# Kernel optimization log

Measured on AMD Instinct MI355X. Metric: run time of the kernel, lower is better.

Reference implementation:

```python
import jax, jax.numpy as jnp
import numpy as np

B, C, H, W = 8, 512, 64, 64
NUMS, V_C = 1024, 512
RATE = 0.999


def _normalize(x):
    # matches torch F.normalize(dim=-1, eps=1e-12)
    return x / jnp.clip(jnp.linalg.norm(x, axis=-1, keepdims=True), 1e-12)


def setup_inputs() -> dict:
    key = jax.random.key(0)
    k1, k2, k3 = jax.random.split(key, 3)
    return {
        "x": jax.random.normal(k1, (B, C, H, W), dtype=jnp.float32),
        "noise_feature": jax.random.normal(k2, (NUMS, C), dtype=jnp.float32),
        "std": jax.random.normal(k3, (NUMS, V_C), dtype=jnp.float32),
    }


def reference(x, noise_feature, std):
    b, c, h, w = x.shape
    # (b,c,h,w) -> (n,c)
    xf = jnp.transpose(x, (0, 2, 3, 1)).reshape(-1, c)
    m = jax.lax.stop_gradient(noise_feature)  # torch uses .data (no grad)
    xn = _normalize(xf)
    mn = _normalize(m)
    score = xn @ mn.T  # (n, k) cosine similarities

    # EMA codebook update (training path, update_flag=True)
    xd = jax.lax.stop_gradient(xf)
    embed_ind = jnp.argmax(score, axis=1)  # (n,)
    # segment_sum == x.T @ one_hot(ind), transposed; avoids dense one-hot GEMM
    embed_sum = jax.ops.segment_sum(xd, embed_ind, num_segments=NUMS)  # (k, c)
    counts = jax.ops.segment_sum(jnp.ones((xd.shape[0],), xd.dtype), embed_ind,
                                 num_segments=NUMS)  # (k,)
    embed_mean = embed_sum / (counts[:, None] + 1e-6)
    new_m = m * RATE + embed_mean * (1.0 - RATE)

    mn2 = _normalize(new_m)
    score2 = xn @ mn2.T  # (n, k)
    soft_label = jax.nn.softmax(score2, axis=1)
    out = (soft_label @ std).reshape(b, h, w, V_C)
    return out, score2
```

## Files before the change

### kernel.cpp

```cpp
#include <hip/hip_runtime.h>
#include <stdint.h>

#define NROWS 32768
#define CDIM  512
#define KCODES 1024
#define VC    512
#define LDP 72

typedef unsigned short u16;
typedef unsigned long long u64;
using bf16x8 = __attribute__((ext_vector_type(8))) __bf16;
using f32x4  = __attribute__((ext_vector_type(4))) float;

__device__ __forceinline__ float bf2f(u16 u){
  union { unsigned int i; float f; } x; x.i = ((unsigned int)u) << 16; return x.f;
}
__device__ __forceinline__ u16 f2bf(float f){
  union { float f; unsigned int i; } x; x.f = f;
  unsigned int u = x.i;
  u += 0x7fffu + ((u >> 16) & 1u);
  return (u16)(u >> 16);
}
__device__ __forceinline__ unsigned int pack2(u16 lo, u16 hi){
  return (unsigned int)lo | ((unsigned int)hi << 16);
}
__device__ __forceinline__ unsigned int fkey(float f){
  unsigned int u = __float_as_uint(f);
  return (u & 0x80000000u) ? ~u : (u | 0x80000000u);
}
__device__ __forceinline__ f32x4 mfma16(bf16x8 a, bf16x8 b, f32x4 c){
  return __builtin_amdgcn_mfma_f32_16x16x32_bf16(a, b, c, 0, 0, 0);
}
__device__ __forceinline__ void gload_lds16(const void* g, void* l){
  __builtin_amdgcn_global_load_lds(
      (const __attribute__((address_space(1))) unsigned int*)g,
      (__attribute__((address_space(3))) unsigned int*)l, 16, 0, 0);
}

__global__ __launch_bounds__(256) void k_transpose_x(const float* __restrict__ x,
                                                     u16* __restrict__ xf){
  __shared__ float tile[32][33];
  int b  = blockIdx.z;
  int p0 = blockIdx.x * 32;
  int c0 = blockIdx.y * 32;
  int tx = threadIdx.x, ty = threadIdx.y;
  const float* xb = x + (size_t)b * CDIM * 4096;
#pragma unroll
  for (int i = 0; i < 4; i++){
    int c = c0 + ty + i * 8;
    tile[ty + i * 8][tx] = xb[(size_t)c * 4096 + p0 + tx];
  }
  __syncthreads();
#pragma unroll
  for (int i = 0; i < 4; i++){
    int p = p0 + ty + i * 8;
    xf[((size_t)(b * 4096 + p)) * CDIM + c0 + tx] = f2bf(tile[tx][ty + i * 8]);
  }
}

__global__ __launch_bounds__(256) void k_rownorm(const u16* __restrict__ xf,
                                                 float* __restrict__ rinv){
  int row  = blockIdx.x * 4 + (threadIdx.x >> 6);
  int lane = threadIdx.x & 63;
  const uint4* p = (const uint4*)(xf + (size_t)row * CDIM);
  uint4 v = p[lane];
  unsigned int w[4] = {v.x, v.y, v.z, v.w};
  float s = 0.f;
#pragma unroll
  for (int i = 0; i < 4; i++){
    float a = bf2f((u16)(w[i] & 0xffffu));
    float b = bf2f((u16)(w[i] >> 16));
    s += a * a + b * b;
  }
#pragma unroll
  for (int off = 32; off; off >>= 1) s += __shfl_xor(s, off, 64);
  if (lane == 0) rinv[row] = 1.0f / fmaxf(sqrtf(s), 1e-12f);
}

__global__ __launch_bounds__(256) void k_norm_rows(const float* __restrict__ in,
                                                   u16* __restrict__ out){
  int row  = blockIdx.x * 4 + (threadIdx.x >> 6);
  int lane = threadIdx.x & 63;
  const float* r = in + (size_t)row * CDIM;
  float v[8]; float s = 0.f;
#pragma unroll
  for (int i = 0; i < 8; i++){ v[i] = r[lane + i * 64]; s += v[i] * v[i]; }
#pragma unroll
  for (int off = 32; off; off >>= 1) s += __shfl_xor(s, off, 64);
  float inv = 1.0f / fmaxf(sqrtf(s), 1e-12f);
#pragma unroll
  for (int i = 0; i < 8; i++) out[(size_t)row * CDIM + lane + i * 64] = f2bf(v[i] * inv);
}

__global__ __launch_bounds__(256) void k_transpose_std(const float* __restrict__ sd,
                                                       u16* __restrict__ stdT){
  __shared__ float tile[32][33];
  int k0 = blockIdx.x * 32;
  int v0 = blockIdx.y * 32;
  int tx = threadIdx.x, ty = threadIdx.y;
#pragma unroll
  for (int i = 0; i < 4; i++)
    tile[ty + i * 8][tx] = sd[(size_t)(k0 + ty + i * 8) * VC + v0 + tx];
  __syncthreads();
#pragma unroll
  for (int i = 0; i < 4; i++)
    stdT[(size_t)(v0 + ty + i * 8) * KCODES + k0 + tx] = f2bf(tile[tx][ty + i * 8]);
}

__global__ __launch_bounds__(256) void k_gemm1_am(const u16* __restrict__ xf,
                                                  const u16* __restrict__ mn,
                                                  u64* __restrict__ packed){
  __shared__ u16 As[128 * 64];
  __shared__ u16 Bs[128 * 64];
  int tid  = threadIdx.x;
  int wave = tid >> 6, lane = tid & 63;
  int wr = wave >> 1, wc = wave & 1;
  int quad = lane >> 4, l15 = lane & 15;
  int c0 = blockIdx.x * 128, r0 = blockIdx.y * 128;

  int srow = lane >> 3, schunk = lane & 7;
  const u16* ag = xf + (size_t)(r0 + wave * 8 + srow) * CDIM + schunk * 8;
  const u16* bg = mn + (size_t)(c0 + wave * 8 + srow) * CDIM + schunk * 8;
  u16* adst = As + wave * 8 * 64;
  u16* bdst = Bs + wave * 8 * 64;

  f32x4 acc[4][4];
#pragma unroll
  for (int rt = 0; rt < 4; rt++)
#pragma unroll
    for (int ct = 0; ct < 4; ct++) acc[rt][ct] = (f32x4)(0.f);

  for (int k0 = 0; k0 < CDIM; k0 += 64){
#pragma unroll
    for (int i = 0; i < 4; i++){
      gload_lds16(ag + (size_t)i * 32 * CDIM + k0, adst + i * 32 * 64);
      gload_lds16(bg + (size_t)i * 32 * CDIM + k0, bdst + i * 32 * 64);
    }
    __syncthreads();
#pragma unroll
    for (int ks = 0; ks < 2; ks++){
      bf16x8 af[4], bfr[4];
#pragma unroll
      for (int rt = 0; rt < 4; rt++)
        af[rt] = *(const bf16x8*)(As + (wr * 64 + rt * 16 + l15) * 64 + ks * 32 + quad * 8);
#pragma unroll
      for (int ct = 0; ct < 4; ct++)
        bfr[ct] = *(const bf16x8*)(Bs + (wc * 64 + ct * 16 + l15) * 64 + ks * 32 + quad * 8);
#pragma unroll
      for (int rt = 0; rt < 4; rt++)
#pragma unroll
        for (int ct = 0; ct < 4; ct++)
          acc[rt][ct] = mfma16(af[rt], bfr[ct], acc[rt][ct]);
    }
    __syncthreads();
  }

#pragma unroll
  for (int rt = 0; rt < 4; rt++){
#pragma unroll
    for (int q = 0; q < 4; q++){
      float bv = acc[rt][0][q];
      int   bc = c0 + wc * 64 + l15;
#pragma unroll
      for (int ct = 1; ct < 4; ct++){
        float v = acc[rt][ct][q];
        int   c = c0 + wc * 64 + ct * 16 + l15;
        if (v > bv){ bv = v; bc = c; }
      }
#pragma unroll
      for (int off = 1; off <= 8; off <<= 1){
        float ov = __shfl_xor(bv, off, 64);
        int   oc = __shfl_xor(bc, off, 64);
        if (ov > bv || (ov == bv && oc < bc)){ bv = ov; bc = oc; }
      }
      if (l15 == 0){
        int rg = r0 + wr * 64 + rt * 16 + quad * 4 + q;
        u64 key = ((u64)fkey(bv) << 32) | (unsigned int)(~(unsigned int)bc);
        atomicMax(packed + rg, key);
      }
    }
  }
}

__global__ __launch_bounds__(256) void k_decode(const u64* __restrict__ packed,
                                                int* __restrict__ ind){
  int i = blockIdx.x * 256 + threadIdx.x;
  ind[i] = (int)(~(unsigned int)(packed[i] & 0xffffffffull)) & (KCODES - 1);
}

__global__ __launch_bounds__(256) void k_gather(const int* __restrict__ ind,
                                                const u16* __restrict__ xf,
                                                float* __restrict__ esum,
                                                float* __restrict__ counts){
  __shared__ float part[4][CDIM];
  __shared__ int   wcnt[4];
  int code = blockIdx.x;
  int tid = threadIdx.x, wave = tid >> 6, lane = tid & 63;
  float acc[8] = {0,0,0,0,0,0,0,0};
  int cnt = 0;
  for (int base = wave * 64; base < NROWS; base += 256){
    int match = (ind[base + lane] == code);
    u64 mask = __ballot(match);
    cnt += (int)__popcll(mask);
    while (mask){
      int b = __ffsll((long long)mask) - 1;
      mask &= mask - 1;
      int rr = base + b;
      uint4 v = *(const uint4*)(xf + (size_t)rr * CDIM + lane * 8);
      unsigned int w[4] = {v.x, v.y, v.z, v.w};
#pragma unroll
      for (int i = 0; i < 4; i++){
        acc[2 * i]     += bf2f((u16)(w[i] & 0xffffu));
        acc[2 * i + 1] += bf2f((u16)(w[i] >> 16));
      }
    }
  }
#pragma unroll
  for (int j = 0; j < 8; j++) part[wave][lane * 8 + j] = acc[j];
  if (lane == 0) wcnt[wave] = cnt;
  __syncthreads();
  for (int c = tid; c < CDIM; c += 256)
    esum[(size_t)code * CDIM + c] = part[0][c] + part[1][c] + part[2][c] + part[3][c];
  if (tid == 0) counts[code] = (float)(wcnt[0] + wcnt[1] + wcnt[2] + wcnt[3]);
}

__global__ __launch_bounds__(256) void k_newm(const float* __restrict__ m,
                                              const float* __restrict__ esum,
                                              const float* __restrict__ counts,
                                              u16* __restrict__ mn2){
  int row  = blockIdx.x * 4 + (threadIdx.x >> 6);
  int lane = threadIdx.x & 63;
  float cnt = counts[row];
  float sc  = 0.001f / (cnt + 1e-6f);
  float v[8]; float s = 0.f;
#pragma unroll
  for (int i = 0; i < 8; i++){
    int c = lane + i * 64;
    v[i] = m[(size_t)row * CDIM + c] * 0.999f + esum[(size_t)row * CDIM + c] * sc;
    s += v[i] * v[i];
  }
#pragma unroll
  for (int off = 32; off; off >>= 1) s += __shfl_xor(s, off, 64);
  float inv = 1.0f / fmaxf(sqrtf(s), 1e-12f);
#pragma unroll
  for (int i = 0; i < 8; i++) mn2[(size_t)row * CDIM + lane + i * 64] = f2bf(v[i] * inv);
}

__global__ __launch_bounds__(256) void k_gemm2(const u16* __restrict__ xf,
                                               const u16* __restrict__ mn2,
                                               const float* __restrict__ rinv,
                                               float* __restrict__ score2,
                                               float* __restrict__ pmax,
                                               float* __restrict__ psum){
  __shared__ u16 As[128 * 64];
  __shared__ u16 Bs[128 * 64];
  int tid  = threadIdx.x;
  int wave = tid >> 6, lane = tid & 63;
  int wr = wave >> 1, wc = wave & 1;
  int quad = lane >> 4, l15 = lane & 15;
  int c0 = blockIdx.x * 128, r0 = blockIdx.y * 128;

  int srow = lane >> 3, schunk = lane & 7;
  const u16* ag = xf  + (size_t)(r0 + wave * 8 + srow) * CDIM + schunk * 8;
  const u16* bg = mn2 + (size_t)(c0 + wave * 8 + srow) * CDIM + schunk * 8;
  u16* adst = As + wave * 8 * 64;
  u16* bdst = Bs + wave * 8 * 64;

  f32x4 acc[4][4];
#pragma unroll
  for (int rt = 0; rt < 4; rt++)
#pragma unroll
    for (int ct = 0; ct < 4; ct++) acc[rt][ct] = (f32x4)(0.f);

  for (int k0 = 0; k0 < CDIM; k0 += 64){
#pragma unroll
    for (int i = 0; i < 4; i++){
      gload_lds16(ag + (size_t)i * 32 * CDIM + k0, adst + i * 32 * 64);
      gload_lds16(bg + (size_t)i * 32 * CDIM + k0, bdst + i * 32 * 64);
    }
    __syncthreads();
#pragma unroll
    for (int ks = 0; ks < 2; ks++){
      bf16x8 af[4], bfr[4];
#pragma unroll
      for (int rt = 0; rt < 4; rt++)
        af[rt] = *(const bf16x8*)(As + (wr * 64 + rt * 16 + l15) * 64 + ks * 32 + quad * 8);
#pragma unroll
      for (int ct = 0; ct < 4; ct++)
        bfr[ct] = *(const bf16x8*)(Bs + (wc * 64 + ct * 16 + l15) * 64 + ks * 32 + quad * 8);
#pragma unroll
      for (int rt = 0; rt < 4; rt++)
#pragma unroll
        for (int ct = 0; ct < 4; ct++)
          acc[rt][ct] = mfma16(af[rt], bfr[ct], acc[rt][ct]);
    }
    __syncthreads();
  }

#pragma unroll
  for (int rt = 0; rt < 4; rt++){
#pragma unroll
    for (int q = 0; q < 4; q++){
      int grow = r0 + wr * 64 + rt * 16 + quad * 4 + q;
      float rv = rinv[grow];
      float v0 = acc[rt][0][q] * rv;
      float v1 = acc[rt][1][q] * rv;
      float v2 = acc[rt][2][q] * rv;
      float v3 = acc[rt][3][q] * rv;
      float* so = score2 + (size_t)grow * KCODES + c0 + wc * 64 + l15;
      so[0]  = v0;
      so[16] = v1;
      so[32] = v2;
      so[48] = v3;
      float mx = fmaxf(fmaxf(v0, v1), fmaxf(v2, v3));
#pragma unroll
      for (int off = 1; off <= 8; off <<= 1) mx = fmaxf(mx, __shfl_xor(mx, off, 64));
      float s = __expf(v0 - mx) + __expf(v1 - mx) + __expf(v2 - mx) + __expf(v3 - mx);
#pragma unroll
      for (int off = 1; off <= 8; off <<= 1) s += __shfl_xor(s, off, 64);
      if (l15 == 0){
        int pi = grow * 16 + blockIdx.x * 2 + wc;
        pmax[pi] = mx;
        psum[pi] = s;
      }
    }
  }
}

__global__ __launch_bounds__(256) void k_softcomb(const float* __restrict__ pmax,
                                                  const float* __restrict__ psum,
                                                  float* __restrict__ rowmax,
                                                  float* __restrict__ rsinv){
  int row = blockIdx.x * 256 + threadIdx.x;
  const float* pm = pmax + (size_t)row * 16;
  const float* ps = psum + (size_t)row * 16;
  float M = pm[0];
#pragma unroll
  for (int i = 1; i < 16; i++) M = fmaxf(M, pm[i]);
  float S = 0.f;
#pragma unroll
  for (int i = 0; i < 16; i++) S += ps[i] * __expf(pm[i] - M);
  rowmax[row] = M;
  rsinv[row]  = 1.0f / S;
}

__global__ __launch_bounds__(512) void k_gemm3(const float* __restrict__ score2,
                                               const float* __restrict__ rowmax,
                                               const float* __restrict__ rsinv,
                                               const u16* __restrict__ stdT,
                                               float* __restrict__ out){
  __shared__ u16 As[128 * LDP];
  __shared__ u16 Bs[256 * 64];
  int tid  = threadIdx.x;
  int wave = tid >> 6, lane = tid & 63;
  int wr = wave >> 2, wcol = wave & 3;
  int quad = lane >> 4, l15 = lane & 15;
  int c0 = blockIdx.x * 256, r0 = blockIdx.y * 128;
  int arow = tid >> 2, aq = tid & 3;

  int srow = lane >> 3, schunk = lane & 7;
  const u16* bg = stdT + (size_t)(c0 + wave * 8 + srow) * KCODES + schunk * 8;
  u16* bdst = Bs + wave * 8 * 64;

  float rmax = rowmax[r0 + arow];
  float rs   = rsinv [r0 + arow];

  f32x4 acc[4][4];
#pragma unroll
  for (int rt = 0; rt < 4; rt++)
#pragma unroll
    for (int ct = 0; ct < 4; ct++) acc[rt][ct] = (f32x4)(0.f);

  const float* ag = score2 + (size_t)(r0 + arow) * KCODES + aq * 16;

  for (int k0 = 0; k0 < KCODES; k0 += 64){
#pragma unroll
    for (int i = 0; i < 4; i++)
      gload_lds16(bg + (size_t)i * 64 * KCODES + k0, bdst + i * 64 * 64);
#pragma unroll
    for (int j = 0; j < 2; j++){
      float4 a = *(const float4*)(ag + k0 + j * 8);
      float4 b = *(const float4*)(ag + k0 + j * 8 + 4);
      uint4 o;
      o.x = pack2(f2bf(__expf(a.x - rmax) * rs), f2bf(__expf(a.y - rmax) * rs));
      o.y = pack2(f2bf(__expf(a.z - rmax) * rs), f2bf(__expf(a.w - rmax) * rs));
      o.z = pack2(f2bf(__expf(b.x - rmax) * rs), f2bf(__expf(b.y - rmax) * rs));
      o.w = pack2(f2bf(__expf(b.z - rmax) * rs), f2bf(__expf(b.w - rmax) * rs));
      *(uint4*)(As + arow * LDP + aq * 16 + j * 8) = o;
    }
    __syncthreads();
#pragma unroll
    for (int ks = 0; ks < 2; ks++){
      bf16x8 af[4], bfr[4];
#pragma unroll
      for (int rt = 0; rt < 4; rt++)
        af[rt] = *(const bf16x8*)(As + (wr * 64 + rt * 16 + l15) * LDP + ks * 32 + quad * 8);
#pragma unroll
      for (int ct = 0; ct < 4; ct++)
        bfr[ct] = *(const bf16x8*)(Bs + (wcol * 64 + ct * 16 + l15) * 64 + ks * 32 + quad * 8);
#pragma unroll
      for (int rt = 0; rt < 4; rt++)
#pragma unroll
        for (int ct = 0; ct < 4; ct++)
          acc[rt][ct] = mfma16(af[rt], bfr[ct], acc[rt][ct]);
    }
    __syncthreads();
  }
#pragma unroll
  for (int rt = 0; rt < 4; rt++){
#pragma unroll
    for (int q = 0; q < 4; q++){
      int grow = r0 + wr * 64 + rt * 16 + quad * 4 + q;
#pragma unroll
      for (int ct = 0; ct < 4; ct++){
        int gcol = c0 + wcol * 64 + ct * 16 + l15;
        out[(size_t)grow * VC + gcol] = acc[rt][ct][q];
      }
    }
  }
}

extern "C" void kernel_launch(void* const* d_in, const int* in_sizes, int n_in,
                              void* d_out, int out_size, void* d_ws, size_t ws_size,
                              hipStream_t stream){
  (void)in_sizes; (void)n_in; (void)out_size; (void)ws_size;
  const float* x      = (const float*)d_in[0];
  const float* m      = (const float*)d_in[1];
  const float* stdmat = (const float*)d_in[2];
  float* out    = (float*)d_out;
  float* score2 = out + (size_t)NROWS * VC;

  char* ws = (char*)d_ws;
  u16*   xf     = (u16*)  (ws + 0);
  u16*   mn     = (u16*)  (ws + 33554432);
  u16*   mn2    = (u16*)  (ws + 34603008);
  u16*   stdT   = (u16*)  (ws + 35651584);
  float* rinv   = (float*)(ws + 36700160);
  u64*   packed = (u64*)  (ws + 36831232);
  int*   ind    = (int*)  (ws + 37093376);
  float* esum   = (float*)(ws + 37224448);
  float* counts = (float*)(ws + 39321600);
  float* rowmax = (float*)(ws + 39325696);
  float* rsinv  = (float*)(ws + 39456768);
  float* pmax   = (float*)(ws + 39587840);
  float* psum   = (float*)(ws + 41684992);

  hipMemsetAsync(packed, 0, (size_t)NROWS * 8, stream);

  k_transpose_x  <<<dim3(128, 16, 8), dim3(32, 8), 0, stream>>>(x, xf);
  k_rownorm      <<<NROWS / 4, 256, 0, stream>>>(xf, rinv);
  k_norm_rows    <<<KCODES / 4, 256, 0, stream>>>(m, mn);
  k_transpose_std<<<dim3(32, 16), dim3(32, 8), 0, stream>>>(stdmat, stdT);
  k_gemm1_am     <<<dim3(KCODES / 128, NROWS / 128), 256, 0, stream>>>(xf, mn, packed);
  k_decode       <<<NROWS / 256, 256, 0, stream>>>(packed, ind);
  k_gather       <<<KCODES, 256, 0, stream>>>(ind, xf, esum, counts);
  k_newm         <<<KCODES / 4, 256, 0, stream>>>(m, esum, counts, mn2);
  k_gemm2        <<<dim3(KCODES / 128, NROWS / 128), 256, 0, stream>>>(xf, mn2, rinv, score2, pmax, psum);
  k_softcomb     <<<NROWS / 256, 256, 0, stream>>>(pmax, psum, rowmax, rsinv);
  k_gemm3        <<<dim3(VC / 256, NROWS / 128), 512, 0, stream>>>(score2, rowmax, rsinv, stdT, out);
}
```

Before: 507.2 us.

## Fuse score GEMM, online softmax and value GEMM into a flash-style kernel

Replaces the separate score GEMM, softmax-combine and softmax@std GEMM kernels with one kernel per 64-row tile. The tile keeps the x rows resident in LDS, streams codebook and std chunks, and applies an online softmax with running max and sum rescaling. This avoids re-reading the 128MB score2 matrix and recomputing exp in a separate pass. The cost is about 145KB of LDS per block, which limits occupancy to one block per CU. The small per-chunk tiles (32 codes) with several barriers per iteration may also underuse the MFMA units.

```diff
diff --git a/kernel.cpp b/kernel.cpp
--- a/kernel.cpp
+++ b/kernel.cpp
@@ -5,7 +5,6 @@
 #define CDIM  512
 #define KCODES 1024
 #define VC    512
-#define LDP 72
 
 typedef unsigned short u16;
 typedef unsigned long long u64;
@@ -246,178 +245,173 @@
   for (int i = 0; i < 8; i++) mn2[(size_t)row * CDIM + lane + i * 64] = f2bf(v[i] * inv);
 }
 
-__global__ __launch_bounds__(256) void k_gemm2(const u16* __restrict__ xf,
+#define SM_AS   0
+#define SM_BS   65536
+#define SM_VS   98304
+#define SM_SF   131072
+#define SM_PT   140288
+#define SM_RM   144384
+#define SM_RL   144640
+#define SM_RS   144896
+__global__ __launch_bounds__(512) void k_fused(const u16* __restrict__ xf,
                                                const u16* __restrict__ mn2,
                                                const float* __restrict__ rinv,
+                                               const u16* __restrict__ stdT,
                                                float* __restrict__ score2,
-                                               float* __restrict__ pmax,
-                                               float* __restrict__ psum){
-  __shared__ u16 As[128 * 64];
-  __shared__ u16 Bs[128 * 64];
+                                               float* __restrict__ out){
+  __shared__ char smem[145152];
+  char* AsB = smem + SM_AS;
+  char* BsB = smem + SM_BS;
+  char* VsB = smem + SM_VS;
+  float* Sf = (float*)(smem + SM_SF);
+  char* PtB = smem + SM_PT;
+  float* rowm = (float*)(smem + SM_RM);
+  float* rowl = (float*)(smem + SM_RL);
+  float* rowsc = (float*)(smem + SM_RS);
+
   int tid  = threadIdx.x;
   int wave = tid >> 6, lane = tid & 63;
-  int wr = wave >> 1, wc = wave & 1;
   int quad = lane >> 4, l15 = lane & 15;
-  int c0 = blockIdx.x * 128, r0 = blockIdx.y * 128;
-
-  int srow = lane >> 3, schunk = lane & 7;
-  const u16* ag = xf  + (size_t)(r0 + wave * 8 + srow) * CDIM + schunk * 8;
-  const u16* bg = mn2 + (size_t)(c0 + wave * 8 + srow) * CDIM + schunk * 8;
-  u16* adst = As + wave * 8 * 64;
-  u16* bdst = Bs + wave * 8 * 64;
-
-  f32x4 acc[4][4];
-#pragma unroll
-  for (int rt = 0; rt < 4; rt++)
-#pragma unroll
-    for (int ct = 0; ct < 4; ct++) acc[rt][ct] = (f32x4)(0.f);
-
-  for (int k0 = 0; k0 < CDIM; k0 += 64){
-#pragma unroll
-    for (int i = 0; i < 4; i++){
-      gload_lds16(ag + (size_t)i * 32 * CDIM + k0, adst + i * 32 * 64);
-      gload_lds16(bg + (size_t)i * 32 * CDIM + k0, bdst + i * 32 * 64);
-    }
-    __syncthreads();
-#pragma unroll
-    for (int ks = 0; ks < 2; ks++){
-      bf16x8 af[4], bfr[4];
-#pragma unroll
-      for (int rt = 0; rt < 4; rt++)
-        af[rt] = *(const bf16x8*)(As + (wr * 64 + rt * 16 + l15) * 64 + ks * 32 + quad * 8);
-#pragma unroll
-      for (int ct = 0; ct < 4; ct++)
-        bfr[ct] = *(const bf16x8*)(Bs + (wc * 64 + ct * 16 + l15) * 64 + ks * 32 + quad * 8);
-#pragma unroll
-      for (int rt = 0; rt < 4; rt++)
-#pragma unroll
-        for (int ct = 0; ct < 4; ct++)
-          acc[rt][ct] = mfma16(af[rt], bfr[ct], acc[rt][ct]);
-    }
-    __syncthreads();
-  }
-
-#pragma unroll
-  for (int rt = 0; rt < 4; rt++){
+  int r0 = blockIdx.x * 64;
+
+  int fr = wave >> 1, fc = wave & 1;
+  int ar = fr * 16 + l15;
+  int br = fc * 16 + l15;
+
+  int wr2 = wave >> 2, wc4 = wave & 3;
+  int R = wr2 * 32, C = wc4 * 128;
+
+  int srow = tid >> 3, ssub = tid & 7;
+  float rv = rinv[r0 + srow];
+
+  f32x4 acc[2][8];
+#pragma unroll
+  for (int rt = 0; rt < 2; rt++)
+#pragma unroll
+    for (int ct = 0; ct < 8; ct++) acc[rt][ct] = (f32x4)(0.f);
+
+#pragma unroll
+  for (int i = 0; i < 8; i++){
+    int rr = wave * 8 + i;
+    gload_lds16(xf + (size_t)(r0 + rr) * CDIM + ((lane ^ (rr & 7)) * 8),
+                AsB + rr * 1024);
+  }
+#pragma unroll
+  for (int i = 0; i < 4; i++){
+    int rr = wave + i * 8;
+    gload_lds16(mn2 + (size_t)rr * CDIM + ((lane ^ (rr & 7)) * 8),
+                BsB + rr * 1024);
+  }
+#pragma unroll
+  for (int i = 0; i < 4; i++){
+    int vb = (wave * 4 + i) * 16;
+    int vc = vb + (lane >> 2);
+    gload_lds16(stdT + (size_t)vc * KCODES + (((lane & 3) ^ (vc & 3)) * 8),
+                VsB + vb * 64);
+  }
+  if (tid < 64){ rowm[tid] = -3.0e38f; rowl[tid] = 0.f; }
+  asm volatile("s_waitcnt vmcnt(0)" ::: "memory");
+  __syncthreads();
+
+  for (int t = 0; t < 32; ++t){
+    int kt = t * 32;
+    f32x4 sacc = (f32x4)(0.f);
+#pragma unroll
+    for (int ks = 0; ks < 16; ++ks){
+      bf16x8 a = *(const bf16x8*)(AsB + ar * 1024 + (((ks * 4 + quad) ^ (ar & 7)) << 4));
+      bf16x8 b = *(const bf16x8*)(BsB + br * 1024 + (((ks * 4 + quad) ^ (br & 7)) << 4));
+      sacc = mfma16(a, b, sacc);
+    }
+#pragma unroll
+    for (int q = 0; q < 4; ++q)
+      Sf[(fr * 16 + quad * 4 + q) * 36 + fc * 16 + l15] = sacc[q];
+    asm volatile("s_waitcnt lgkmcnt(0)" ::: "memory");
+    __builtin_amdgcn_s_barrier();
+    if (t + 1 < 32){
+#pragma unroll
+      for (int i = 0; i < 4; i++){
+        int rr = wave + i * 8;
+        gload_lds16(mn2 + (size_t)(kt + 32 + rr) * CDIM + ((lane ^ (rr & 7)) * 8),
+                    BsB + rr * 1024);
+      }
+    }
+    {
+      f32x4 v = *(const f32x4*)(Sf + srow * 36 + ssub * 4);
+      v *= rv;
+      *(f32x4*)(score2 + (size_t)(r0 + srow) * KCODES + kt + ssub * 4) = v;
+      float mx = fmaxf(fmaxf(v[0], v[1]), fmaxf(v[2], v[3]));
+      mx = fmaxf(mx, __shfl_xor(mx, 1, 64));
+      mx = fmaxf(mx, __shfl_xor(mx, 2, 64));
+      mx = fmaxf(mx, __shfl_xor(mx, 4, 64));
+      float mo = rowm[srow];
+      float mn_ = fmaxf(mo, mx);
+      float d = __expf(mo - mn_);
+      float p0 = __expf(v[0] - mn_), p1 = __expf(v[1] - mn_);
+      float p2 = __expf(v[2] - mn_), p3 = __expf(v[3] - mn_);
+      float ss = p0 + p1 + p2 + p3;
+      ss += __shfl_xor(ss, 1, 64);
+      ss += __shfl_xor(ss, 2, 64);
+      ss += __shfl_xor(ss, 4, 64);
+      if (ssub == 0){
+        rowl[srow] = rowl[srow] * d + ss;
+        rowm[srow] = mn_;
+        rowsc[srow] = d;
+      }
+      uint2 pw;
+      pw.x = pack2(f2bf(p0), f2bf(p1));
+      pw.y = pack2(f2bf(p2), f2bf(p3));
+      *(uint2*)(PtB + srow * 64 + (((ssub >> 1) ^ (srow & 3)) << 4) + ((ssub & 1) << 3)) = pw;
+    }
+    asm volatile("s_waitcnt vmcnt(4) lgkmcnt(0)" ::: "memory");
+    __builtin_amdgcn_s_barrier();
+    __builtin_amdgcn_sched_barrier(0);
+#pragma unroll
+    for (int rt = 0; rt < 2; rt++)
+#pragma unroll
+      for (int q = 0; q < 4; q++){
+        float s = rowsc[R + rt * 16 + quad * 4 + q];
+#pragma unroll
+        for (int ct = 0; ct < 8; ct++) acc[rt][ct][q] *= s;
+      }
+    bf16x8 pa[2];
+#pragma unroll
+    for (int rt = 0; rt < 2; rt++){
+      int rr = R + rt * 16 + l15;
+      pa[rt] = *(const bf16x8*)(PtB + rr * 64 + ((quad ^ (rr & 3)) << 4));
+    }
+#pragma unroll
+    for (int ct = 0; ct < 8; ct++){
+      int vc = C + ct * 16 + l15;
+      bf16x8 bv = *(const bf16x8*)(VsB + vc * 64 + ((quad ^ (vc & 3)) << 4));
+#pragma unroll
+      for (int rt = 0; rt < 2; rt++) acc[rt][ct] = mfma16(pa[rt], bv, acc[rt][ct]);
+    }
+    asm volatile("s_waitcnt lgkmcnt(0)" ::: "memory");
+    __builtin_amdgcn_s_barrier();
+    if (t + 1 < 32){
+#pragma unroll
+      for (int i = 0; i < 4; i++){
+        int vb = (wave * 4 + i) * 16;
+        int vc = vb + (lane >> 2);
+        gload_lds16(stdT + (size_t)vc * KCODES + kt + 32 + (((lane & 3) ^ (vc & 3)) * 8),
+                    VsB + vb * 64);
+      }
+      asm volatile("s_waitcnt vmcnt(4)" ::: "memory");
+      __builtin_amdgcn_s_barrier();
+      __builtin_amdgcn_sched_barrier(0);
+    }
+  }
+
+#pragma unroll
+  for (int rt = 0; rt < 2; rt++)
 #pragma unroll
     for (int q = 0; q < 4; q++){
-      int grow = r0 + wr * 64 + rt * 16 + quad * 4 + q;
-      float rv = rinv[grow];
-      float v0 = acc[rt][0][q] * rv;
-      float v1 = acc[rt][1][q] * rv;
-      float v2 = acc[rt][2][q] * rv;
-      float v3 = acc[rt][3][q] * rv;
-      float* so = score2 + (size_t)grow * KCODES + c0 + wc * 64 + l15;
-      so[0]  = v0;
-      so[16] = v1;
-      so[32] = v2;
-      so[48] = v3;
-      float mx = fmaxf(fmaxf(v0, v1), fmaxf(v2, v3));
-#pragma unroll
-      for (int off = 1; off <= 8; off <<= 1) mx = fmaxf(mx, __shfl_xor(mx, off, 64));
-      float s = __expf(v0 - mx) + __expf(v1 - mx) + __expf(v2 - mx) + __expf(v3 - mx);
-#pragma unroll
-      for (int off = 1; off <= 8; off <<= 1) s += __shfl_xor(s, off, 64);
-      if (l15 == 0){
-        int pi = grow * 16 + blockIdx.x * 2 + wc;
-        pmax[pi] = mx;
-        psum[pi] = s;
-      }
-    }
-  }
-}
-
-__global__ __launch_bounds__(256) void k_softcomb(const float* __restrict__ pmax,
-                                                  const float* __restrict__ psum,
-                                                  float* __restrict__ rowmax,
-                                                  float* __restrict__ rsinv){
-  int row = blockIdx.x * 256 + threadIdx.x;
-  const float* pm = pmax + (size_t)row * 16;
-  const float* ps = psum + (size_t)row * 16;
-  float M = pm[0];
-#pragma unroll
-  for (int i = 1; i < 16; i++) M = fmaxf(M, pm[i]);
-  float S = 0.f;
-#pragma unroll
-  for (int i = 0; i < 16; i++) S += ps[i] * __expf(pm[i] - M);
-  rowmax[row] = M;
-  rsinv[row]  = 1.0f / S;
-}
-
-__global__ __launch_bounds__(512) void k_gemm3(const float* __restrict__ score2,
-                                               const float* __restrict__ rowmax,
-                                               const float* __restrict__ rsinv,
-                                               const u16* __restrict__ stdT,
-                                               float* __restrict__ out){
-  __shared__ u16 As[128 * LDP];
-  __shared__ u16 Bs[256 * 64];
-  int tid  = threadIdx.x;
-  int wave = tid >> 6, lane = tid & 63;
-  int wr = wave >> 2, wcol = wave & 3;
-  int quad = lane >> 4, l15 = lane & 15;
-  int c0 = blockIdx.x * 256, r0 = blockIdx.y * 128;
-  int arow = tid >> 2, aq = tid & 3;
-
-  int srow = lane >> 3, schunk = lane & 7;
-  const u16* bg = stdT + (size_t)(c0 + wave * 8 + srow) * KCODES + schunk * 8;
-  u16* bdst = Bs + wave * 8 * 64;
-
-  float rmax = rowmax[r0 + arow];
-  float rs   = rsinv [r0 + arow];
-
-  f32x4 acc[4][4];
-#pragma unroll
-  for (int rt = 0; rt < 4; rt++)
-#pragma unroll
-    for (int ct = 0; ct < 4; ct++) acc[rt][ct] = (f32x4)(0.f);
-
-  const float* ag = score2 + (size_t)(r0 + arow) * KCODES + aq * 16;
-
-  for (int k0 = 0; k0 < KCODES; k0 += 64){
-#pragma unroll
-    for (int i = 0; i < 4; i++)
-      gload_lds16(bg + (size_t)i * 64 * KCODES + k0, bdst + i * 64 * 64);
-#pragma unroll
-    for (int j = 0; j < 2; j++){
-      float4 a = *(const float4*)(ag + k0 + j * 8);
-      float4 b = *(const float4*)(ag + k0 + j * 8 + 4);
-      uint4 o;
-      o.x = pack2(f2bf(__expf(a.x - rmax) * rs), f2bf(__expf(a.y - rmax) * rs));
-      o.y = pack2(f2bf(__expf(a.z - rmax) * rs), f2bf(__expf(a.w - rmax) * rs));
-      o.z = pack2(f2bf(__expf(b.x - rmax) * rs), f2bf(__expf(b.y - rmax) * rs));
-      o.w = pack2(f2bf(__expf(b.z - rmax) * rs), f2bf(__expf(b.w - rmax) * rs));
-      *(uint4*)(As + arow * LDP + aq * 16 + j * 8) = o;
-    }
-    __syncthreads();
-#pragma unroll
-    for (int ks = 0; ks < 2; ks++){
-      bf16x8 af[4], bfr[4];
-#pragma unroll
-      for (int rt = 0; rt < 4; rt++)
-        af[rt] = *(const bf16x8*)(As + (wr * 64 + rt * 16 + l15) * LDP + ks * 32 + quad * 8);
-#pragma unroll
-      for (int ct = 0; ct < 4; ct++)
-        bfr[ct] = *(const bf16x8*)(Bs + (wcol * 64 + ct * 16 + l15) * 64 + ks * 32 + quad * 8);
-#pragma unroll
-      for (int rt = 0; rt < 4; rt++)
-#pragma unroll
-        for (int ct = 0; ct < 4; ct++)
-          acc[rt][ct] = mfma16(af[rt], bfr[ct], acc[rt][ct]);
-    }
-    __syncthreads();
-  }
-#pragma unroll
-  for (int rt = 0; rt < 4; rt++){
-#pragma unroll
-    for (int q = 0; q < 4; q++){
-      int grow = r0 + wr * 64 + rt * 16 + quad * 4 + q;
-#pragma unroll
-      for (int ct = 0; ct < 4; ct++){
-        int gcol = c0 + wcol * 64 + ct * 16 + l15;
-        out[(size_t)grow * VC + gcol] = acc[rt][ct][q];
-      }
-    }
-  }
+      int rr = R + rt * 16 + quad * 4 + q;
+      float inv = 1.0f / rowl[rr];
+#pragma unroll
+      for (int ct = 0; ct < 8; ct++)
+        out[(size_t)(r0 + rr) * VC + C + ct * 16 + l15] = acc[rt][ct][q] * inv;
+    }
 }
 
 extern "C" void kernel_launch(void* const* d_in, const int* in_sizes, int n_in,
@@ -440,10 +434,6 @@
   int*   ind    = (int*)  (ws + 37093376);
   float* esum   = (float*)(ws + 37224448);
   float* counts = (float*)(ws + 39321600);
-  float* rowmax = (float*)(ws + 39325696);
-  float* rsinv  = (float*)(ws + 39456768);
-  float* pmax   = (float*)(ws + 39587840);
-  float* psum   = (float*)(ws + 41684992);
 
   hipMemsetAsync(packed, 0, (size_t)NROWS * 8, stream);
 
@@ -455,7 +445,5 @@
   k_decode       <<<NROWS / 256, 256, 0, stream>>>(packed, ind);
   k_gather       <<<KCODES, 256, 0, stream>>>(ind, xf, esum, counts);
   k_newm         <<<KCODES / 4, 256, 0, stream>>>(m, esum, counts, mn2);
-  k_gemm2        <<<dim3(KCODES / 128, NROWS / 128), 256, 0, stream>>>(xf, mn2, rinv, score2, pmax, psum);
-  k_softcomb     <<<NROWS / 256, 256, 0, stream>>>(pmax, psum, rowmax, rsinv);
-  k_gemm3        <<<dim3(VC / 256, NROWS / 128), 512, 0, stream>>>(score2, rowmax, rsinv, stdT, out);
-}
+  k_fused        <<<NROWS / 64, 512, 0, stream>>>(xf, mn2, rinv, stdT, score2, out);
+}
```

After: 541.3 us. 1.07x slower.

## Fuse row-norm into vectorized transpose and fold argmax decode into gather

Applied to the files above, without the earlier changes.

The x transpose now uses 64x64 tiles with float4 loads, an XOR-swizzled LDS layout and 16-byte bf16 stores. It also computes per-row sum of squares, accumulating the 8 channel-tile partials through atomicAdd into a zeroed buffer, and a tiny kernel finalizes the inverse norm. This removes the separate k_rownorm pass that re-read xf. The decode kernel is removed, and the gather kernel decodes packed argmax keys directly. The trade-offs are an extra memset, float atomics with nondeterministic summation order, and reading 8-byte keys in every gather block.

```diff
diff --git a/kernel.cpp b/kernel.cpp
--- a/kernel.cpp
+++ b/kernel.cpp
@@ -38,43 +38,51 @@
 }
 
 __global__ __launch_bounds__(256) void k_transpose_x(const float* __restrict__ x,
-                                                     u16* __restrict__ xf){
-  __shared__ float tile[32][33];
+                                                     u16* __restrict__ xf,
+                                                     float* __restrict__ rsum){
+  __shared__ float tile[64 * 64];
   int b  = blockIdx.z;
-  int p0 = blockIdx.x * 32;
-  int c0 = blockIdx.y * 32;
-  int tx = threadIdx.x, ty = threadIdx.y;
-  const float* xb = x + (size_t)b * CDIM * 4096;
+  int p0 = blockIdx.x * 64;
+  int c0 = blockIdx.y * 64;
+  int t  = threadIdx.x;
+  const float* xb = x + (size_t)b * CDIM * 4096 + (size_t)c0 * 4096 + p0;
+
+  int pl4 = (t & 15) * 4;
 #pragma unroll
   for (int i = 0; i < 4; i++){
-    int c = c0 + ty + i * 8;
-    tile[ty + i * 8][tx] = xb[(size_t)c * 4096 + p0 + tx];
+    int cl = i * 16 + (t >> 4);
+    float4 v = *(const float4*)(xb + (size_t)cl * 4096 + pl4);
+    *(float4*)(tile + cl * 64 + (pl4 ^ (cl & 0x38))) = v;
   }
   __syncthreads();
-#pragma unroll
-  for (int i = 0; i < 4; i++){
-    int p = p0 + ty + i * 8;
-    xf[((size_t)(b * 4096 + p)) * CDIM + c0 + tx] = f2bf(tile[tx][ty + i * 8]);
-  }
-}
-
-__global__ __launch_bounds__(256) void k_rownorm(const u16* __restrict__ xf,
-                                                 float* __restrict__ rinv){
-  int row  = blockIdx.x * 4 + (threadIdx.x >> 6);
-  int lane = threadIdx.x & 63;
-  const uint4* p = (const uint4*)(xf + (size_t)row * CDIM);
-  uint4 v = p[lane];
-  unsigned int w[4] = {v.x, v.y, v.z, v.w};
-  float s = 0.f;
-#pragma unroll
-  for (int i = 0; i < 4; i++){
-    float a = bf2f((u16)(w[i] & 0xffffu));
-    float b = bf2f((u16)(w[i] >> 16));
-    s += a * a + b * b;
-  }
-#pragma unroll
-  for (int off = 32; off; off >>= 1) s += __shfl_xor(s, off, 64);
-  if (lane == 0) rinv[row] = 1.0f / fmaxf(sqrtf(s), 1e-12f);
+
+  int cl0 = (t & 7) * 8;
+#pragma unroll
+  for (int pass = 0; pass < 2; pass++){
+    int pl = pass * 32 + (t >> 3);
+    float v[8]; float s = 0.f;
+#pragma unroll
+    for (int j = 0; j < 8; j++){
+      v[j] = tile[(cl0 + j) * 64 + (pl ^ cl0)];
+      s += v[j] * v[j];
+    }
+    uint4 o;
+    o.x = pack2(f2bf(v[0]), f2bf(v[1]));
+    o.y = pack2(f2bf(v[2]), f2bf(v[3]));
+    o.z = pack2(f2bf(v[4]), f2bf(v[5]));
+    o.w = pack2(f2bf(v[6]), f2bf(v[7]));
+    *(uint4*)(xf + (size_t)(b * 4096 + p0 + pl) * CDIM + c0 + cl0) = o;
+    s += __shfl_xor(s, 1, 64);
+    s += __shfl_xor(s, 2, 64);
+    s += __shfl_xor(s, 4, 64);
+    if ((t & 7) == 0) atomicAdd(rsum + b * 4096 + p0 + pl, s);
+  }
+}
+
+__global__ __launch_bounds__(256) void k_rinv_fin(const float* __restrict__ rsum,
+                                                  float* __restrict__ rinv){
+  int i = blockIdx.x * 256 + threadIdx.x;
+  rinv[i] = 1.0f / fmaxf(sqrtf(rsum[i]), 1e-12f);
 }
 
 __global__ __launch_bounds__(256) void k_norm_rows(const float* __restrict__ in,
@@ -110,8 +118,8 @@
 __global__ __launch_bounds__(256) void k_gemm1_am(const u16* __restrict__ xf,
                                                   const u16* __restrict__ mn,
                                                   u64* __restrict__ packed){
-  __shared__ u16 As[128 * 64];
-  __shared__ u16 Bs[128 * 64];
+  __shared__ __align__(16) u16 As[128 * 64];
+  __shared__ __align__(16) u16 Bs[128 * 64];
   int tid  = threadIdx.x;
   int wave = tid >> 6, lane = tid & 63;
   int wr = wave >> 1, wc = wave & 1;
@@ -182,13 +190,7 @@
   }
 }
 
-__global__ __launch_bounds__(256) void k_decode(const u64* __restrict__ packed,
-                                                int* __restrict__ ind){
-  int i = blockIdx.x * 256 + threadIdx.x;
-  ind[i] = (int)(~(unsigned int)(packed[i] & 0xffffffffull)) & (KCODES - 1);
-}
-
-__global__ __launch_bounds__(256) void k_gather(const int* __restrict__ ind,
+__global__ __launch_bounds__(256) void k_gather(const u64* __restrict__ packed,
                                                 const u16* __restrict__ xf,
                                                 float* __restrict__ esum,
                                                 float* __restrict__ counts){
@@ -199,7 +201,9 @@
   float acc[8] = {0,0,0,0,0,0,0,0};
   int cnt = 0;
   for (int base = wave * 64; base < NROWS; base += 256){
-    int match = (ind[base + lane] == code);
+    u64 pk = packed[base + lane];
+    int cl = (int)(~(unsigned int)(pk & 0xffffffffull)) & (KCODES - 1);
+    int match = (cl == code);
     u64 mask = __ballot(match);
     cnt += (int)__popcll(mask);
     while (mask){
@@ -252,8 +256,8 @@
                                                float* __restrict__ score2,
                                                float* __restrict__ pmax,
                                                float* __restrict__ psum){
-  __shared__ u16 As[128 * 64];
-  __shared__ u16 Bs[128 * 64];
+  __shared__ __align__(16) u16 As[128 * 64];
+  __shared__ __align__(16) u16 Bs[128 * 64];
   int tid  = threadIdx.x;
   int wave = tid >> 6, lane = tid & 63;
   int wr = wave >> 1, wc = wave & 1;
@@ -349,8 +353,8 @@
                                                const float* __restrict__ rsinv,
                                                const u16* __restrict__ stdT,
                                                float* __restrict__ out){
-  __shared__ u16 As[128 * LDP];
-  __shared__ u16 Bs[256 * 64];
+  __shared__ __align__(16) u16 As[128 * LDP];
+  __shared__ __align__(16) u16 Bs[256 * 64];
   int tid  = threadIdx.x;
   int wave = tid >> 6, lane = tid & 63;
   int wr = wave >> 2, wcol = wave & 3;
@@ -437,23 +441,23 @@
   u16*   stdT   = (u16*)  (ws + 35651584);
   float* rinv   = (float*)(ws + 36700160);
   u64*   packed = (u64*)  (ws + 36831232);
-  int*   ind    = (int*)  (ws + 37093376);
   float* esum   = (float*)(ws + 37224448);
   float* counts = (float*)(ws + 39321600);
   float* rowmax = (float*)(ws + 39325696);
   float* rsinv  = (float*)(ws + 39456768);
   float* pmax   = (float*)(ws + 39587840);
   float* psum   = (float*)(ws + 41684992);
+  float* rsum   = rowmax;
 
   hipMemsetAsync(packed, 0, (size_t)NROWS * 8, stream);
-
-  k_transpose_x  <<<dim3(128, 16, 8), dim3(32, 8), 0, stream>>>(x, xf);
-  k_rownorm      <<<NROWS / 4, 256, 0, stream>>>(xf, rinv);
+  hipMemsetAsync(rsum,   0, (size_t)NROWS * 4, stream);
+
+  k_transpose_x  <<<dim3(64, 8, 8), 256, 0, stream>>>(x, xf, rsum);
+  k_rinv_fin     <<<NROWS / 256, 256, 0, stream>>>(rsum, rinv);
   k_norm_rows    <<<KCODES / 4, 256, 0, stream>>>(m, mn);
   k_transpose_std<<<dim3(32, 16), dim3(32, 8), 0, stream>>>(stdmat, stdT);
   k_gemm1_am     <<<dim3(KCODES / 128, NROWS / 128), 256, 0, stream>>>(xf, mn, packed);
-  k_decode       <<<NROWS / 256, 256, 0, stream>>>(packed, ind);
-  k_gather       <<<KCODES, 256, 0, stream>>>(ind, xf, esum, counts);
+  k_gather       <<<KCODES, 256, 0, stream>>>(packed, xf, esum, counts);
   k_newm         <<<KCODES / 4, 256, 0, stream>>>(m, esum, counts, mn2);
   k_gemm2        <<<dim3(KCODES / 128, NROWS / 128), 256, 0, stream>>>(xf, mn2, rinv, score2, pmax, psum);
   k_softcomb     <<<NROWS / 256, 256, 0, stream>>>(pmax, psum, rowmax, rsinv);
```

New measurement: 503.0 us. Within noise of the previous version (-0.8%).
